# Kernel optimization log

Measured on AMD Instinct MI355X. Metric: run time of the kernel, lower is better.

Reference implementation:

```python
import jax, jax.numpy as jnp
import numpy as np

ALPHA = 1.0
ARAP_WEIGHT = 1.0
B, N, K, LATENT, HIDDEN = 16, 20000, 16, 256, 1024


def setup_inputs() -> dict:
    key = jax.random.key(0)
    ks = jax.random.split(key, 8)
    code = jax.random.normal(ks[0], (B, LATENT), jnp.float32)
    W1 = jax.random.normal(ks[1], (LATENT, HIDDEN), jnp.float32) / np.sqrt(LATENT)
    b1 = jnp.zeros((HIDDEN,), jnp.float32)
    W2 = jax.random.normal(ks[2], (HIDDEN, N * 3), jnp.float32) / np.sqrt(HIDDEN)
    b2 = jnp.zeros((N * 3,), jnp.float32)
    xyz1 = jax.random.normal(ks[3], (B, N, 3), jnp.float32)
    weightMatrix = jax.random.uniform(ks[4], (N, K), jnp.float32)
    area = jax.random.uniform(ks[5], (N,), jnp.float32)
    neighborsMatrix = jax.random.randint(ks[6], (N, K), 0, N, jnp.int32)
    numNeighbors = jax.random.randint(ks[7], (N,), 1, K + 1, jnp.int32)
    return {"code": code, "W1": W1, "b1": b1, "W2": W2, "b2": b2,
            "xyz1": xyz1, "weightMatrix": weightMatrix, "area": area,
            "neighborsMatrix": neighborsMatrix, "numNeighbors": numNeighbors}


def _mean_energy(code, W1, b1, W2, b2, xyz1, weightMatrix, area,
                 neighborsMatrix, numNeighbors):
    # decoder: MLP latent -> hidden -> N*3, reshaped to [B,N,3]
    h = jax.nn.relu(code @ W1 + b1)
    recon = (h @ W2 + b2).reshape(B, N, 3)

    # mask out padded neighbor slots, fold into weights  [N,K]
    mask = (jnp.arange(K)[None, :] < numNeighbors[:, None]).astype(jnp.float32)
    wm = weightMatrix * mask

    # neighbor-gathered edge vectors: rest pose d, deformed dq  [B,N,K,3]
    d = xyz1[:, :, None, :] - xyz1[:, neighborsMatrix, :]
    dq = recon[:, :, None, :] - recon[:, neighborsMatrix, :]

    # per-vertex weighted covariance and best-fit rotation (Procrustes)
    S = jnp.einsum('nk,bnki,bnkj->bnij', wm, d, dq)          # [B,N,3,3]
    U, s, Vt = jnp.linalg.svd(S)
    V = jnp.swapaxes(Vt, -1, -2)
    Ut = jnp.swapaxes(U, -1, -2)
    det = jnp.linalg.det(V @ Ut)                              # [B,N]
    Vf = V.at[..., :, -1].multiply(jnp.sign(det)[..., None])  # reflection fix
    R = jax.lax.stop_gradient(Vf @ Ut)                        # R treated as constant

    resid = dq - jnp.einsum('bnij,bnkj->bnki', R, d)          # [B,N,K,3]
    e = (ARAP_WEIGHT * ALPHA) * area[None, :, None] * wm[None] \
        * jnp.sum(resid * resid, axis=-1)                     # [B,N,K]
    # torch.mean(torch.mean(e, 2), 1)
    return jnp.mean(e, axis=(1, 2))                           # [B]


def reference(code, W1, b1, W2, b2, xyz1, weightMatrix, area,
              neighborsMatrix, numNeighbors):
    meanEnergy = _mean_energy(code, W1, b1, W2, b2, xyz1, weightMatrix, area,
                              neighborsMatrix, numNeighbors)
    # meanEnergy.backward(ones) -> grad of sum(meanEnergy) wrt code
    code_grad = jax.grad(lambda c: jnp.sum(
        _mean_energy(c, W1, b1, W2, b2, xyz1, weightMatrix, area,
                     neighborsMatrix, numNeighbors)))(code)
    return (meanEnergy, code_grad)
```

## Files before the change

### kernel.cpp

```cpp
#include <hip/hip_runtime.h>

constexpr int B_ = 16;
constexpr int NV = 20000;
constexpr int KN = 16;
constexpr int LAT = 256;
constexpr int HID = 1024;
constexpr int N3 = 60000;
constexpr int RCAP = 64;
constexpr int NCHUNK = 8;
constexpr float INV_NK = 1.0f / (20000.0f * 16.0f);

constexpr size_t H_OFF      = 0;
constexpr size_t XQ_OFF     = H_OFF + B_ * HID;
constexpr size_t GRECON_OFF = XQ_OFF + (size_t)NV * 96;
constexpr size_t GH_OFF     = GRECON_OFF + (size_t)B_ * N3;
constexpr size_t OWNG_OFF   = GH_OFF + B_ * HID;
constexpr size_t GEDGE_OFF  = OWNG_OFF + (size_t)NV * 64;
constexpr size_t RCOUNT_OFF = GEDGE_OFF + (size_t)NV * KN * 64;
constexpr size_t RLIST_OFF  = RCOUNT_OFF + NV;
constexpr size_t PART_OFF   = RLIST_OFF + (size_t)NV * RCAP;

__device__ __forceinline__ void atomAddF(float* p, float v) {
  unsafeAtomicAdd(p, v);
}

__global__ __launch_bounds__(256) void k_prep(
    const float* __restrict__ xyz, const float* __restrict__ code,
    const float* __restrict__ W1, const float* __restrict__ b1,
    float* __restrict__ xq, float* __restrict__ h,
    float* __restrict__ gh, float* __restrict__ out,
    int* __restrict__ rcount) {
  const int bid = blockIdx.x, tid = threadIdx.x;
  if (bid < 938) {
    __shared__ float sm[64][17];
    const int n30 = bid * 64;
    {
      const int n3l = tid & 63, bq = tid >> 6;
      #pragma unroll
      for (int p = 0; p < 4; ++p) {
        int b = p * 4 + bq;
        if (n30 + n3l < N3) sm[n3l][b] = xyz[(size_t)b * N3 + n30 + n3l];
      }
    }
    __syncthreads();
    {
      const int b = tid & 15, nq = tid >> 4;
      #pragma unroll
      for (int p = 0; p < 4; ++p) {
        int n3 = n30 + p * 16 + nq;
        if (n3 < N3) {
          int n = n3 / 3, c = n3 - n * 3;
          xq[(size_t)n * 96 + c * 16 + b] = sm[p * 16 + nq][b];
        }
      }
    }
  } else if (bid < 1002) {
    int t = (bid - 938) * 256 + tid;
    int b = t >> 10, hd = t & 1023;
    const float* c = code + b * LAT;
    float acc = b1[hd];
    #pragma unroll 4
    for (int l = 0; l < LAT; ++l) acc += c[l] * W1[l * HID + hd];
    h[t] = fmaxf(acc, 0.0f);
  } else if (bid < 1006) {
    int base = (bid - 1002) * 4096 + tid;
    #pragma unroll
    for (int r = 0; r < 16; ++r) gh[base + r * 256] = 0.0f;
  } else if (bid == 1006) {
    for (int i = tid; i < B_ + B_ * LAT; i += 256) out[i] = 0.0f;
  } else {
    int i = (bid - 1007) * 256 + tid;
    if (i < NV) rcount[i] = 0;
  }
}

__global__ __launch_bounds__(256) void k_mlp2f(
    const float* __restrict__ h, const float* __restrict__ W2,
    float* __restrict__ part,
    const int* __restrict__ nbrs, const int* __restrict__ nnbr,
    int* __restrict__ rcount, int* __restrict__ rlist) {
  const int bid = blockIdx.x;
  const int tid = threadIdx.x;
  if (bid >= 472) {
    int e = (bid - 472) * 256 + tid;
    int n = e >> 4, k = e & 15;
    if (k < nnbr[n]) {
      int v = nbrs[e];
      int slot = atomicAdd(&rcount[v], 1);
      if (slot < RCAP) rlist[v * RCAP + slot] = e;
    }
    return;
  }
  const int bx = bid % 59, by = bid / 59;
  __shared__ float hs[16][128];
  const int hd0 = by * 128;
  #pragma unroll
  for (int r = 0; r < 8; ++r) {
    int idx = r * 256 + tid;
    int bb = idx >> 7, cc = idx & 127;
    hs[bb][cc] = h[bb * HID + hd0 + cc];
  }
  __syncthreads();

  const int j4 = bx * 1024 + tid * 4;
  if (j4 >= N3) return;

  float4 acc[16];
  #pragma unroll
  for (int b = 0; b < 16; ++b) acc[b] = make_float4(0.f, 0.f, 0.f, 0.f);

  const float* wp = W2 + (size_t)hd0 * N3 + j4;
  float4 w0 = *(const float4*)(wp);
  float4 w1 = *(const float4*)(wp + (size_t)N3);
  float4 w2 = *(const float4*)(wp + (size_t)2 * N3);
  float4 w3 = *(const float4*)(wp + (size_t)3 * N3);

  for (int g = 0; g < 32; ++g) {
    const float* np = wp + (size_t)4 * N3;
    float4 n0, n1, n2, n3;
    if (g < 31) {
      n0 = *(const float4*)(np);
      n1 = *(const float4*)(np + (size_t)N3);
      n2 = *(const float4*)(np + (size_t)2 * N3);
      n3 = *(const float4*)(np + (size_t)3 * N3);
    }
    #pragma unroll
    for (int b = 0; b < 16; ++b) {
      float4 hb = *(const float4*)&hs[b][g * 4];
      acc[b].x += hb.x * w0.x + hb.y * w1.x + hb.z * w2.x + hb.w * w3.x;
      acc[b].y += hb.x * w0.y + hb.y * w1.y + hb.z * w2.y + hb.w * w3.y;
      acc[b].z += hb.x * w0.z + hb.y * w1.z + hb.z * w2.z + hb.w * w3.z;
      acc[b].w += hb.x * w0.w + hb.y * w1.w + hb.z * w2.w + hb.w * w3.w;
    }
    wp = np; w0 = n0; w1 = n1; w2 = n2; w3 = n3;
  }

  float ac[4][16];
  #pragma unroll
  for (int b = 0; b < 16; ++b) {
    ac[0][b] = acc[b].x; ac[1][b] = acc[b].y;
    ac[2][b] = acc[b].z; ac[3][b] = acc[b].w;
  }
  float* pbase = part + ((size_t)by * N3 + j4) * 16;
  #pragma unroll
  for (int jj = 0; jj < 4; ++jj)
    #pragma unroll
    for (int q = 0; q < 4; ++q)
      *(float4*)(pbase + jj * 16 + q * 4) = make_float4(
          ac[jj][q*4+0], ac[jj][q*4+1], ac[jj][q*4+2], ac[jj][q*4+3]);
}

__global__ __launch_bounds__(256) void k_reduce(
    const float* __restrict__ part, const float* __restrict__ b2,
    float* __restrict__ xq) {
  int t = blockIdx.x * 256 + threadIdx.x;
  if (t >= N3 * 16 / 4) return;
  size_t pos = (size_t)t * 4;
  int j = t >> 2, bq = (t & 3) * 4;
  float4 s = *(const float4*)(part + pos);
  #pragma unroll
  for (int c = 1; c < NCHUNK; ++c) {
    float4 p = *(const float4*)(part + (size_t)c * N3 * 16 + pos);
    s.x += p.x; s.y += p.y; s.z += p.z; s.w += p.w;
  }
  float bias = b2[j];
  s.x += bias; s.y += bias; s.z += bias; s.w += bias;
  int n = j / 3, c = j - n * 3;
  *(float4*)(xq + (size_t)n * 96 + (3 + c) * 16 + bq) = s;
}

__global__ __launch_bounds__(256, 4) void k_rot(
    const float* __restrict__ xq,
    const float* __restrict__ wmat, const float* __restrict__ area,
    const int* __restrict__ nbrs, const int* __restrict__ nnbr,
    float* __restrict__ ownG, float* __restrict__ gEdge,
    float* __restrict__ energy) {
  __shared__ float red[64];
  const int tid = threadIdx.x;
  const int b = tid & 15, nl = tid >> 4;
  const int n = blockIdx.x * 16 + nl;
  const int nn = nnbr[n];
  const float ar = area[n];
  const float* xqn = xq + (size_t)n * 96 + b;
  const float x0 = xqn[0],  x1 = xqn[16], x2 = xqn[32];
  const float q0 = xqn[48], q1 = xqn[64], q2 = xqn[80];

  float S00=0,S01=0,S02=0,S10=0,S11=0,S12=0,S20=0,S21=0,S22=0;
  #pragma unroll
  for (int k = 0; k < KN; ++k) {
    if (k < nn) {
      int m = nbrs[n * KN + k];
      float w = wmat[n * KN + k];
      const float* mp = xq + (size_t)m * 96 + b;
      float dx = x0 - mp[0],  dy = x1 - mp[16], dz = x2 - mp[32];
      float ex = q0 - mp[48], ey = q1 - mp[64], ez = q2 - mp[80];
      S00 += w*dx*ex; S01 += w*dx*ey; S02 += w*dx*ez;
      S10 += w*dy*ex; S11 += w*dy*ey; S12 += w*dy*ez;
      S20 += w*dz*ex; S21 += w*dz*ey; S22 += w*dz*ez;
    }
  }

  float A00 = S00*S00 + S10*S10 + S20*S20;
  float A01 = S00*S01 + S10*S11 + S20*S21;
  float A02 = S00*S02 + S10*S12 + S20*S22;
  float A11 = S01*S01 + S11*S11 + S21*S21;
  float A12 = S01*S02 + S11*S12 + S21*S22;
  float A22 = S02*S02 + S12*S12 + S22*S22;
  float V00=1,V01=0,V02=0, V10=0,V11=1,V12=0, V20=0,V21=0,V22=1;

  auto rot = [&](float& app, float& aqq, float& apq, float& arp, float& arq,
                 float& vp0, float& vp1, float& vp2,
                 float& vq0, float& vq1, float& vq2) {
    float a = apq;
    if (fabsf(a) > 1e-37f) {
      float tau = (aqq - app) * 0.5f / a;
      float t = copysignf(1.0f, tau) / (fabsf(tau) + sqrtf(1.0f + tau * tau));
      float c = rsqrtf(1.0f + t * t);
      float s = t * c;
      float napp = c*c*app - 2.0f*s*c*a + s*s*aqq;
      float naqq = s*s*app + 2.0f*s*c*a + c*c*aqq;
      app = napp; aqq = naqq; apq = 0.0f;
      float rp = arp, rq = arq;
      arp = c*rp - s*rq; arq = s*rp + c*rq;
      float t0, t1;
      t0=vp0; t1=vq0; vp0 = c*t0 - s*t1; vq0 = s*t0 + c*t1;
      t0=vp1; t1=vq1; vp1 = c*t0 - s*t1; vq1 = s*t0 + c*t1;
      t0=vp2; t1=vq2; vp2 = c*t0 - s*t1; vq2 = s*t0 + c*t1;
    }
  };
  #pragma unroll
  for (int sweep = 0; sweep < 6; ++sweep) {
    rot(A00,A11,A01, A02,A12, V00,V10,V20, V01,V11,V21);
    rot(A00,A22,A02, A01,A12, V00,V10,V20, V02,V12,V22);
    rot(A11,A22,A12, A01,A02, V01,V11,V21, V02,V12,V22);
  }
  auto sw = [](float& a, float& c) { float t = a; a = c; c = t; };
  if (A00 < A11) { sw(A00,A11); sw(V00,V01); sw(V10,V11); sw(V20,V21); }
  if (A00 < A22) { sw(A00,A22); sw(V00,V02); sw(V10,V12); sw(V20,V22); }
  if (A11 < A22) { sw(A11,A22); sw(V01,V02); sw(V11,V12); sw(V21,V22); }

  float v1x=V00, v1y=V10, v1z=V20;
  float v2x=V01, v2y=V11, v2z=V21;

  float u1x = S00*v1x + S01*v1y + S02*v1z;
  float u1y = S10*v1x + S11*v1y + S12*v1z;
  float u1z = S20*v1x + S21*v1y + S22*v1z;
  float s1sq = u1x*u1x + u1y*u1y + u1z*u1z;
  if (s1sq > 1e-30f) { float r = rsqrtf(s1sq); u1x*=r; u1y*=r; u1z*=r; }
  else { u1x = 1.0f; u1y = 0.0f; u1z = 0.0f; }

  float u2x = S00*v2x + S01*v2y + S02*v2z;
  float u2y = S10*v2x + S11*v2y + S12*v2z;
  float u2z = S20*v2x + S21*v2y + S22*v2z;
  float pr = u2x*u1x + u2y*u1y + u2z*u1z;
  u2x -= pr*u1x; u2y -= pr*u1y; u2z -= pr*u1z;
  float s2sq = u2x*u2x + u2y*u2y + u2z*u2z;
  if (s2sq > 1e-12f * s1sq + 1e-30f) {
    float r = rsqrtf(s2sq); u2x*=r; u2y*=r; u2z*=r;
  } else {
    float ex_ = (fabsf(u1x) < 0.9f) ? 1.0f : 0.0f;
    float ey_ = 1.0f - ex_;
    float pp = ex_*u1x + ey_*u1y;
    u2x = ex_ - pp*u1x; u2y = ey_ - pp*u1y; u2z = -pp*u1z;
    float r = rsqrtf(u2x*u2x + u2y*u2y + u2z*u2z);
    u2x*=r; u2y*=r; u2z*=r;
  }
  float u3x = u1y*u2z - u1z*u2y, u3y = u1z*u2x - u1x*u2z, u3z = u1x*u2y - u1y*u2x;
  float v3x = v1y*v2z - v1z*v2y, v3y = v1z*v2x - v1x*v2z, v3z = v1x*v2y - v1y*v2x;

  float R00 = v1x*u1x + v2x*u2x + v3x*u3x;
  float R01 = v1x*u1y + v2x*u2y + v3x*u3y;
  float R02 = v1x*u1z + v2x*u2z + v3x*u3z;
  float R10 = v1y*u1x + v2y*u2x + v3y*u3x;
  float R11 = v1y*u1y + v2y*u2y + v3y*u3y;
  float R12 = v1y*u1z + v2y*u2z + v3y*u3z;
  float R20 = v1z*u1x + v2z*u2x + v3z*u3x;
  float R21 = v1z*u1y + v2z*u2y + v3z*u3y;
  float R22 = v1z*u1z + v2z*u2z + v3z*u3z;

  float esum = 0, go0 = 0, go1 = 0, go2 = 0;
  const float gf = 2.0f * ar * INV_NK;
  float* geb = gEdge + (size_t)n * 1024 + b * 4;
  #pragma unroll
  for (int k = 0; k < KN; ++k) {
    if (k < nn) {
      int m = nbrs[n * KN + k];
      float w = wmat[n * KN + k];
      const float* mp = xq + (size_t)m * 96 + b;
      float dx = x0 - mp[0],  dy = x1 - mp[16], dz = x2 - mp[32];
      float ex = q0 - mp[48], ey = q1 - mp[64], ez = q2 - mp[80];
      float rx = ex - (R00*dx + R01*dy + R02*dz);
      float ry = ey - (R10*dx + R11*dy + R12*dz);
      float rz = ez - (R20*dx + R21*dy + R22*dz);
      esum += w * (rx*rx + ry*ry + rz*rz);
      float gc = gf * w;
      float gx = gc*rx, gy = gc*ry, gz = gc*rz;
      go0 += gx; go1 += gy; go2 += gz;
      *(float4*)(geb + k * 64) = make_float4(gx, gy, gz, 0.0f);
    }
  }
  esum *= ar * INV_NK;

  *(float4*)(ownG + (size_t)n * 64 + b * 4) = make_float4(go0, go1, go2, 0.0f);

  esum += __shfl_down(esum, 32);
  esum += __shfl_down(esum, 16);
  int wave = tid >> 6, lane = tid & 63;
  if (lane < 16) red[wave * 16 + lane] = esum;
  __syncthreads();
  if (tid < 16) atomAddF(&energy[tid], red[tid] + red[16 + tid] + red[32 + tid] + red[48 + tid]);
}

__global__ __launch_bounds__(256) void k_scatter(
    const float* __restrict__ gEdge, const float* __restrict__ ownG,
    const int* __restrict__ rcount, const int* __restrict__ rlist,
    float* __restrict__ grecon) {
  int t = blockIdx.x * 256 + threadIdx.x;
  int v = t >> 4, b = t & 15;
  const float4 og = *(const float4*)(ownG + (size_t)v * 64 + b * 4);
  float g0 = og.x, g1 = og.y, g2 = og.z;
  int deg = min(rcount[v], RCAP);
  const int* rl = rlist + v * RCAP;
  int i = 0;
  for (; i + 3 < deg; i += 4) {
    int e0 = rl[i], e1 = rl[i + 1], e2 = rl[i + 2], e3 = rl[i + 3];
    float4 p0 = *(const float4*)(gEdge + (size_t)e0 * 64 + b * 4);
    float4 p1 = *(const float4*)(gEdge + (size_t)e1 * 64 + b * 4);
    float4 p2 = *(const float4*)(gEdge + (size_t)e2 * 64 + b * 4);
    float4 p3 = *(const float4*)(gEdge + (size_t)e3 * 64 + b * 4);
    g0 -= (p0.x + p1.x) + (p2.x + p3.x);
    g1 -= (p0.y + p1.y) + (p2.y + p3.y);
    g2 -= (p0.z + p1.z) + (p2.z + p3.z);
  }
  for (; i < deg; ++i) {
    int e = rl[i];
    float4 p = *(const float4*)(gEdge + (size_t)e * 64 + b * 4);
    g0 -= p.x; g1 -= p.y; g2 -= p.z;
  }
  float* gq = grecon + (size_t)b * N3 + v * 3;
  gq[0] = g0; gq[1] = g1; gq[2] = g2;
}

__global__ __launch_bounds__(256, 2) void k_mlp2_bwd(
    const float* __restrict__ gr, const float* __restrict__ W2,
    float* __restrict__ gh) {
  const int tid = threadIdx.x;
  const int lane = tid & 63;
  const int wv = tid >> 6;
  const int laneJ = lane & 15, laneR = lane >> 4;
  const int row0 = blockIdx.y * 32 + wv * 8 + laneR * 2;

  float4 acc0[16], acc1[16];
  #pragma unroll
  for (int b = 0; b < 16; ++b) {
    acc0[b] = make_float4(0.f, 0.f, 0.f, 0.f);
    acc1[b] = make_float4(0.f, 0.f, 0.f, 0.f);
  }

  const int jbase = blockIdx.x * 64 + laneJ * 4;
  const float* w2r0 = W2 + (size_t)row0 * N3;
  const float* w2r1 = W2 + (size_t)(row0 + 1) * N3;

  for (int it = 0; it < 59; ++it) {
    int j = jbase + it * 1024;
    if (j < N3) {
      float4 w0 = *(const float4*)(w2r0 + j);
      float4 w1 = *(const float4*)(w2r1 + j);
      #pragma unroll
      for (int b = 0; b < 16; ++b) {
        float4 g = *(const float4*)(gr + (size_t)b * N3 + j);
        acc0[b].x += g.x * w0.x; acc0[b].y += g.y * w0.y;
        acc0[b].z += g.z * w0.z; acc0[b].w += g.w * w0.w;
        acc1[b].x += g.x * w1.x; acc1[b].y += g.y * w1.y;
        acc1[b].z += g.z * w1.z; acc1[b].w += g.w * w1.w;
      }
    }
  }

  float s0[16], s1[16];
  #pragma unroll
  for (int b = 0; b < 16; ++b) {
    s0[b] = (acc0[b].x + acc0[b].y) + (acc0[b].z + acc0[b].w);
    s1[b] = (acc1[b].x + acc1[b].y) + (acc1[b].z + acc1[b].w);
  }
  #pragma unroll
  for (int m = 1; m <= 8; m <<= 1) {
    #pragma unroll
    for (int b = 0; b < 16; ++b) {
      s0[b] += __shfl_xor(s0[b], m);
      s1[b] += __shfl_xor(s1[b], m);
    }
  }
  if (laneJ == 0) {
    #pragma unroll
    for (int b = 0; b < 16; ++b) {
      atomAddF(&gh[b * HID + row0], s0[b]);
      atomAddF(&gh[b * HID + row0 + 1], s1[b]);
    }
  }
}

__global__ __launch_bounds__(256) void k_mlp1_bwd(
    const float* __restrict__ gh, const float* __restrict__ h,
    const float* __restrict__ W1, float* __restrict__ gcode) {
  __shared__ float gm[128];
  const int b = blockIdx.x;
  const int hd0 = blockIdx.y * 128;
  const int l = threadIdx.x;
  if (l < 128) {
    float g = gh[b * HID + hd0 + l];
    gm[l] = (h[b * HID + hd0 + l] > 0.0f) ? g : 0.0f;
  }
  __syncthreads();
  const float4* wp = (const float4*)(W1 + (size_t)l * HID + hd0);
  float acc = 0.0f;
  #pragma unroll
  for (int i = 0; i < 32; ++i) {
    float4 w4 = wp[i];
    acc += w4.x * gm[i*4+0] + w4.y * gm[i*4+1] + w4.z * gm[i*4+2] + w4.w * gm[i*4+3];
  }
  atomAddF(&gcode[b * LAT + l], acc);
}

extern "C" void kernel_launch(void* const* d_in, const int* in_sizes, int n_in,
                              void* d_out, int out_size, void* d_ws, size_t ws_size,
                              hipStream_t stream) {
  const float* code = (const float*)d_in[0];
  const float* W1   = (const float*)d_in[1];
  const float* b1   = (const float*)d_in[2];
  const float* W2   = (const float*)d_in[3];
  const float* b2   = (const float*)d_in[4];
  const float* xyz  = (const float*)d_in[5];
  const float* wmat = (const float*)d_in[6];
  const float* area = (const float*)d_in[7];
  const int* nbrs   = (const int*)d_in[8];
  const int* nnbr   = (const int*)d_in[9];

  float* out = (float*)d_out;
  float* ws = (float*)d_ws;
  float* h      = ws + H_OFF;
  float* xq     = ws + XQ_OFF;
  float* grecon = ws + GRECON_OFF;
  float* gh     = ws + GH_OFF;
  float* ownG   = ws + OWNG_OFF;
  float* gEdge  = ws + GEDGE_OFF;
  int*   rcount = (int*)(ws + RCOUNT_OFF);
  int*   rlist  = (int*)(ws + RLIST_OFF);
  float* part   = ws + PART_OFF;

  k_prep<<<dim3(1086), dim3(256), 0, stream>>>(xyz, code, W1, b1, xq, h, gh, out, rcount);
  k_mlp2f<<<dim3(472 + NV * KN / 256), dim3(256), 0, stream>>>(
      h, W2, part, nbrs, nnbr, rcount, rlist);
  k_reduce<<<dim3((N3 * 16 / 4 + 255) / 256), dim3(256), 0, stream>>>(part, b2, xq);
  k_rot<<<dim3(NV / 16), dim3(256), 0, stream>>>(
      xq, wmat, area, nbrs, nnbr, ownG, gEdge, out);
  k_scatter<<<dim3(NV * 16 / 256), dim3(256), 0, stream>>>(
      gEdge, ownG, rcount, rlist, grecon);
  k_mlp2_bwd<<<dim3(16, 32), dim3(256), 0, stream>>>(grecon, W2, gh);
  k_mlp1_bwd<<<dim3(B_, 8), dim3(256), 0, stream>>>(gh, h, W1, out + B_);
}
```

Baseline: 563.4 us.

## Prefetch W2 into cache during prep and scatter kernels with extra blocks

Adds extra blocks to k_prep and k_scatter that stream the whole 240MB W2 matrix and write a dummy sum into the part workspace. The aim is to warm the large last-level cache (Infinity Cache) so the following W2-heavy GEMM kernels (k_mlp2f, k_mlp2_bwd) read W2 from cache instead of HBM. W2 is larger than the cache, so the prefetch mostly adds HBM traffic. Writing the dump into part before k_mlp2f fills it should be harmless if k_mlp2f overwrites part, but the dump written in k_scatter could collide with whatever part holds at that point.

```diff
diff --git a/kernel.cpp b/kernel.cpp
--- a/kernel.cpp
+++ b/kernel.cpp
@@ -10,6 +10,9 @@
 constexpr int NCHUNK = 8;
 constexpr float INV_NK = 1.0f / (20000.0f * 16.0f);
 
+constexpr int NT = 938;
+constexpr size_t W2_F4 = 15360000;
+
 constexpr size_t H_OFF      = 0;
 constexpr size_t XQ_OFF     = H_OFF + B_ * HID;
 constexpr size_t GRECON_OFF = XQ_OFF + (size_t)NV * 96;
@@ -24,12 +27,30 @@
   unsafeAtomicAdd(p, v);
 }
 
+__device__ __forceinline__ void touchW2(const float* __restrict__ W2,
+                                        float* __restrict__ dump,
+                                        int tb, int tid) {
+  const float4* w4 = (const float4*)W2;
+  float s = 0.0f;
+  size_t base = (size_t)tb * 16384 + tid;
+  #pragma unroll 8
+  for (int i = 0; i < 64; ++i) {
+    size_t idx = base + (size_t)i * 256;
+    if (idx < W2_F4) {
+      float4 v = w4[idx];
+      s += v.x + v.y + v.z + v.w;
+    }
+  }
+  dump[tb * 256 + tid] = s;
+}
+
 __global__ __launch_bounds__(256) void k_prep(
     const float* __restrict__ xyz, const float* __restrict__ code,
     const float* __restrict__ W1, const float* __restrict__ b1,
+    const float* __restrict__ W2,
     float* __restrict__ xq, float* __restrict__ h,
     float* __restrict__ gh, float* __restrict__ out,
-    int* __restrict__ rcount) {
+    int* __restrict__ rcount, float* __restrict__ dump) {
   const int bid = blockIdx.x, tid = threadIdx.x;
   if (bid < 938) {
     __shared__ float sm[64][17];
@@ -68,9 +89,11 @@
     for (int r = 0; r < 16; ++r) gh[base + r * 256] = 0.0f;
   } else if (bid == 1006) {
     for (int i = tid; i < B_ + B_ * LAT; i += 256) out[i] = 0.0f;
-  } else {
+  } else if (bid < 1086) {
     int i = (bid - 1007) * 256 + tid;
     if (i < NV) rcount[i] = 0;
+  } else {
+    touchW2(W2, dump, bid - 1086, tid);
   }
 }
 
@@ -314,8 +337,15 @@
 __global__ __launch_bounds__(256) void k_scatter(
     const float* __restrict__ gEdge, const float* __restrict__ ownG,
     const int* __restrict__ rcount, const int* __restrict__ rlist,
+    const float* __restrict__ W2, float* __restrict__ dump,
     float* __restrict__ grecon) {
-  int t = blockIdx.x * 256 + threadIdx.x;
+  const int bid = blockIdx.x;
+  const int tid = threadIdx.x;
+  if (bid >= 1250) {
+    touchW2(W2, dump, bid - 1250, tid);
+    return;
+  }
+  int t = bid * 256 + tid;
   int v = t >> 4, b = t & 15;
   const float4 og = *(const float4*)(ownG + (size_t)v * 64 + b * 4);
   float g0 = og.x, g1 = og.y, g2 = og.z;
@@ -448,14 +478,15 @@
   int*   rlist  = (int*)(ws + RLIST_OFF);
   float* part   = ws + PART_OFF;
 
-  k_prep<<<dim3(1086), dim3(256), 0, stream>>>(xyz, code, W1, b1, xq, h, gh, out, rcount);
+  k_prep<<<dim3(1086 + NT), dim3(256), 0, stream>>>(
+      xyz, code, W1, b1, W2, xq, h, gh, out, rcount, part);
   k_mlp2f<<<dim3(472 + NV * KN / 256), dim3(256), 0, stream>>>(
       h, W2, part, nbrs, nnbr, rcount, rlist);
   k_reduce<<<dim3((N3 * 16 / 4 + 255) / 256), dim3(256), 0, stream>>>(part, b2, xq);
   k_rot<<<dim3(NV / 16), dim3(256), 0, stream>>>(
       xq, wmat, area, nbrs, nnbr, ownG, gEdge, out);
-  k_scatter<<<dim3(NV * 16 / 256), dim3(256), 0, stream>>>(
-      gEdge, ownG, rcount, rlist, grecon);
+  k_scatter<<<dim3(NV * 16 / 256 + NT), dim3(256), 0, stream>>>(
+      gEdge, ownG, rcount, rlist, W2, part, grecon);
   k_mlp2_bwd<<<dim3(16, 32), dim3(256), 0, stream>>>(grecon, W2, gh);
   k_mlp1_bwd<<<dim3(B_, 8), dim3(256), 0, stream>>>(gh, h, W1, out + B_);
 }
```

Result: slower. 607.5 us (+7.8%).
